# Kernel tuning notes

Hardware: AMD Instinct MI355X
Metric: run time of the kernel (lower is better)

## Reference

```python
import jax, jax.numpy as jnp
import numpy as np

DIMS = [3, 64, 64, 64, 3]  # [input_dim] + hidden dims + [input_dim]
TOTAL_W = sum(DIMS[l] * DIMS[l + 1] + 4 * DIMS[l + 1] for l in range(len(DIMS) - 1))  # 9356


def setup_inputs() -> dict:
    key = jax.random.key(0)
    k1, k2, k3 = jax.random.split(key, 3)
    B, N = 64, 8192
    context = jax.random.normal(k1, (B, N), dtype=jnp.float32)
    y = jax.random.normal(k2, (B, N, DIMS[0]), dtype=jnp.float32)
    tnw = jax.random.normal(k3, (B, TOTAL_W), dtype=jnp.float32) * 0.1
    return {"context": context, "y": y, "target_networks_weights": tnw}


def reference(context, y, target_networks_weights):
    B = target_networks_weights.shape[0]
    dx = y  # [B, N, dims[0]]
    i = 0
    n_layers = len(DIMS) - 1
    for l in range(n_layers):
        dl, dl1 = DIMS[l], DIMS[l + 1]
        W = target_networks_weights[:, i:i + dl * dl1].reshape(B, dl, dl1)
        i += dl * dl1
        bias = target_networks_weights[:, i:i + dl1]          # [B, dl1]
        i += dl1
        w_scale = target_networks_weights[:, i:i + dl1]        # [B, dl1]
        i += dl1
        b_scale = target_networks_weights[:, i:i + dl1]        # [B, dl1]
        i += dl1
        w_shift = target_networks_weights[:, i:i + dl1]        # [B, dl1]
        i += dl1
        # batched matmul + bias
        dx = jnp.einsum('bnd,bde->bne', dx, W) + bias[:, None, :]
        # sigmoid gate: bmm(context[:, :, None], w_scale[:, None, :]) = outer product
        scale = jax.nn.sigmoid(context[:, :, None] * w_scale[:, None, :] + b_scale[:, None, :])
        dx = scale * dx
        # shift term
        dx = dx + context[:, :, None] * w_shift[:, None, :]
        if l < n_layers - 1:
            dx = jax.nn.softplus(dx)
    return dx
```

## Files before the change

### kernel.cpp

```cpp
#include <hip/hip_runtime.h>
#include <math.h>

#define BB 64
#define NN 8192
#define TOTAL_W 9356

typedef _Float16 f16x8 __attribute__((ext_vector_type(8)));
typedef float f32x4 __attribute__((ext_vector_type(4)));
typedef float f32x2 __attribute__((ext_vector_type(2)));
typedef unsigned int u32x2 __attribute__((ext_vector_type(2)));

#define L2E 1.44269504088896340736f
#define LN2 0.6931471805599453f

#define W0_OFF   0
#define FILM_OFF 768
#define A1_OFF   (FILM_OFF + 4096)
#define A2_OFF   (A1_OFF + 8192)
#define ACT_OFF  (A2_OFF + 8192)
#define LDS_BYTES (ACT_OFF + 256*128)

#define MFMA16(a, b, c) __builtin_amdgcn_mfma_f32_16x16x32_f16(a, b, c, 0, 0, 0)
#define EXP2 __builtin_amdgcn_exp2f
#define LOG2 __builtin_amdgcn_logf
#define RCPF __builtin_amdgcn_rcpf

__device__ __forceinline__ f32x2 pfma(f32x2 a, f32x2 b, f32x2 c) {
  return __builtin_elementwise_fma(a, b, c);
}

__device__ __forceinline__ f32x4 filmq(const unsigned char* smem, int l, int prm, int q) {
  return *(const f32x4*)(smem + FILM_OFF + (((l * 4 + prm) * 64 + q) << 2));
}

template<bool SP>
__device__ __forceinline__ u32x2 film_quad(f32x4 acc, float ctx,
                                           f32x4 wscq, f32x4 bscq, f32x4 wshq) {
  f32x2 ctx2 = {ctx, ctx};
  f32x2 one = {1.f, 1.f};
  f32x2 z0 = pfma(ctx2, (f32x2){wscq.x, wscq.y}, (f32x2){bscq.x, bscq.y});
  f32x2 z1 = pfma(ctx2, (f32x2){wscq.z, wscq.w}, (f32x2){bscq.z, bscq.w});
  f32x2 d0 = {EXP2(-z0.x), EXP2(-z0.y)};  d0 += one;
  f32x2 d1 = {EXP2(-z1.x), EXP2(-z1.y)};  d1 += one;
  f32x2 s0 = {RCPF(d0.x), RCPF(d0.y)};
  f32x2 s1 = {RCPF(d1.x), RCPF(d1.y)};
  f32x2 v0 = pfma(ctx2, (f32x2){wshq.x, wshq.y}, s0 * (f32x2){acc.x, acc.y});
  f32x2 v1 = pfma(ctx2, (f32x2){wshq.z, wshq.w}, s1 * (f32x2){acc.z, acc.w});
  if (SP) {
    f32x2 l2 = {L2E, L2E}, ln = {LN2, LN2};
    f32x2 t0 = v0 * l2, t1 = v1 * l2;
    f32x2 u0 = {EXP2(t0.x), EXP2(t0.y)};  u0 += one;
    f32x2 u1 = {EXP2(t1.x), EXP2(t1.y)};  u1 += one;
    f32x2 g0 = {LOG2(u0.x), LOG2(u0.y)};
    f32x2 g1 = {LOG2(u1.x), LOG2(u1.y)};
    v0 = g0 * ln;
    v1 = g1 * ln;
  }
  auto p01 = __builtin_amdgcn_cvt_pkrtz(v0.x, v0.y);
  auto p23 = __builtin_amdgcn_cvt_pkrtz(v1.x, v1.y);
  u32x2 w;
  w.x = __builtin_bit_cast(unsigned int, p01);
  w.y = __builtin_bit_cast(unsigned int, p23);
  return w;
}

__device__ __forceinline__ void act_store(unsigned char* smem, int pt, int slot, u32x2 w) {
  int pos = ((((slot >> 1) ^ (pt & 7)) << 1) | (slot & 1));
  *(u32x2*)(smem + ACT_OFF + pt * 128 + (pos << 3)) = w;
}
__device__ __forceinline__ f16x8 act_load(const unsigned char* smem, int pt, int pair) {
  int gr = pair ^ (pt & 7);
  return *(const f16x8*)(smem + ACT_OFF + pt * 128 + (gr << 4));
}

__global__ __launch_bounds__(512, 6)
void ode_hypernet_kernel(const float* __restrict__ context,
                         const float* __restrict__ y,
                         const float* __restrict__ tnw,
                         float* __restrict__ out) {
  __shared__ __align__(16) unsigned char smem[LDS_BYTES];
  const int b = blockIdx.y;
  const int tid = threadIdx.x;
  const float* __restrict__ wb = tnw + (size_t)b * TOTAL_W;

  if (tid < 192) ((float*)(smem + W0_OFF))[tid] = wb[tid];
  if (tid < 64) {
    const int biaso[4] = {192, 4544, 8896, 9344};
    const int dim[4] = {64, 64, 64, 3};
#pragma unroll
    for (int l = 0; l < 4; ++l) {
      float bv = 0.f, wscv = 0.f, bscv = 0.f, wshv = 0.f;
      if (tid < dim[l]) {
        int bo = biaso[l], d = dim[l];
        bv = wb[bo + tid];
        wscv = wb[bo + d + tid] * L2E;
        bscv = wb[bo + 2 * d + tid] * L2E;
        wshv = wb[bo + 3 * d + tid];
      }
      float* f = (float*)(smem + FILM_OFF) + l * 256;
      f[tid] = bv;
      f[64 + tid] = wscv;
      f[128 + tid] = bscv;
      f[192 + tid] = wshv;
    }
  }
#pragma unroll
  for (int L = 0; L < 2; ++L) {
    const int woff = L ? 4800 : 448;
    const int aoff = L ? A2_OFF : A1_OFF;
#pragma unroll
    for (int it = 0; it < 2; ++it) {
      int idx = tid + it * 512;
      int f_in = idx >> 4;
      int q = idx & 15;
      f32x4 w4 = *(const f32x4*)(wb + woff + f_in * 64 + q * 4);
      int m = q >> 2;
      int c4 = (q & 3) * 4;
      int t = f_in >> 5;
      int h = (f_in >> 3) & 3;
      int i = f_in & 7;
      unsigned char* base = smem + aoff + (m * 128 + t * 64 + h * 16 + c4) * 16 + i * 2;
#pragma unroll
      for (int j = 0; j < 4; ++j)
        *(_Float16*)(base + j * 16) = (_Float16)w4[j];
    }
  }
  const int lane = tid & 63;
  const int colA = lane & 15;
  const int hA = lane >> 4;
  f16x8 A3r0, A3r1;
#pragma unroll
  for (int i = 0; i < 8; ++i) {
    A3r0[i] = (colA < 3) ? (_Float16)wb[9152 + (8 * hA + i) * 3 + colA] : (_Float16)0.f;
    A3r1[i] = (colA < 3) ? (_Float16)wb[9152 + (32 + 8 * hA + i) * 3 + colA] : (_Float16)0.f;
  }
  __syncthreads();

  const int wid = tid >> 6;
  const int g = lane >> 4;
  const int col = lane & 15;
  const int pt0 = wid * 32 + col;
  const int pt1 = pt0 + 16;
  const int q4 = 4 * g;

#pragma unroll 1
  for (int ss = 0; ss < 2; ++ss) {
    const int nbase = blockIdx.x * 512 + ss * 256;
    const int n0 = nbase + pt0, n1 = nbase + pt1;
    const float ctx0 = context[(size_t)b * NN + n0];
    const float ctx1 = context[(size_t)b * NN + n1];
    const size_t yb0 = ((size_t)b * NN + n0) * 3;
    const size_t yb1 = ((size_t)b * NN + n1) * 3;
    const float y00 = y[yb0], y01 = y[yb0 + 1], y02 = y[yb0 + 2];
    const float y10 = y[yb1], y11 = y[yb1 + 1], y12 = y[yb1 + 2];

#pragma unroll
    for (int m = 0; m < 4; ++m) {
      const int q = 16 * m + q4;
      f32x4 biasq = filmq(smem, 0, 0, q);
      f32x4 w0a = *(const f32x4*)(smem + W0_OFF + ((0 * 64 + q) << 2));
      f32x4 w0b = *(const f32x4*)(smem + W0_OFF + ((1 * 64 + q) << 2));
      f32x4 w0c = *(const f32x4*)(smem + W0_OFF + ((2 * 64 + q) << 2));
      f32x2 aLo, aHi, cLo, cHi;
      aLo = pfma((f32x2){y00, y00}, (f32x2){w0a.x, w0a.y}, (f32x2){biasq.x, biasq.y});
      aLo = pfma((f32x2){y01, y01}, (f32x2){w0b.x, w0b.y}, aLo);
      aLo = pfma((f32x2){y02, y02}, (f32x2){w0c.x, w0c.y}, aLo);
      aHi = pfma((f32x2){y00, y00}, (f32x2){w0a.z, w0a.w}, (f32x2){biasq.z, biasq.w});
      aHi = pfma((f32x2){y01, y01}, (f32x2){w0b.z, w0b.w}, aHi);
      aHi = pfma((f32x2){y02, y02}, (f32x2){w0c.z, w0c.w}, aHi);
      cLo = pfma((f32x2){y10, y10}, (f32x2){w0a.x, w0a.y}, (f32x2){biasq.x, biasq.y});
      cLo = pfma((f32x2){y11, y11}, (f32x2){w0b.x, w0b.y}, cLo);
      cLo = pfma((f32x2){y12, y12}, (f32x2){w0c.x, w0c.y}, cLo);
      cHi = pfma((f32x2){y10, y10}, (f32x2){w0a.z, w0a.w}, (f32x2){biasq.z, biasq.w});
      cHi = pfma((f32x2){y11, y11}, (f32x2){w0b.z, w0b.w}, cHi);
      cHi = pfma((f32x2){y12, y12}, (f32x2){w0c.z, w0c.w}, cHi);
      f32x4 acc0 = {aLo.x, aLo.y, aHi.x, aHi.y};
      f32x4 acc1 = {cLo.x, cLo.y, cHi.x, cHi.y};
      f32x4 wscq = filmq(smem, 0, 1, q);
      f32x4 bscq = filmq(smem, 0, 2, q);
      f32x4 wshq = filmq(smem, 0, 3, q);
      act_store(smem, pt0, 4 * m + g, film_quad<true>(acc0, ctx0, wscq, bscq, wshq));
      act_store(smem, pt1, 4 * m + g, film_quad<true>(acc1, ctx1, wscq, bscq, wshq));
    }

#pragma unroll
    for (int L = 1; L <= 2; ++L) {
      const int aoff = (L == 1) ? A1_OFF : A2_OFF;
      f16x8 B00 = act_load(smem, pt0, g);
      f16x8 B01 = act_load(smem, pt0, 4 + g);
      f16x8 B10 = act_load(smem, pt1, g);
      f16x8 B11 = act_load(smem, pt1, 4 + g);
#pragma unroll
      for (int m = 0; m < 4; ++m) {
        const int q = 16 * m + q4;
        f32x4 biasq = filmq(smem, L, 0, q);
        f16x8 a0 = *(const f16x8*)(smem + aoff + ((m * 2 + 0) * 64 + lane) * 16);
        f16x8 a1 = *(const f16x8*)(smem + aoff + ((m * 2 + 1) * 64 + lane) * 16);
        f32x4 c0 = biasq, c1 = biasq;
        c0 = MFMA16(a0, B00, c0);
        c0 = MFMA16(a1, B01, c0);
        c1 = MFMA16(a0, B10, c1);
        c1 = MFMA16(a1, B11, c1);
        f32x4 wscq = filmq(smem, L, 1, q);
        f32x4 bscq = filmq(smem, L, 2, q);
        f32x4 wshq = filmq(smem, L, 3, q);
        act_store(smem, pt0, 4 * m + g, film_quad<true>(c0, ctx0, wscq, bscq, wshq));
        act_store(smem, pt1, 4 * m + g, film_quad<true>(c1, ctx1, wscq, bscq, wshq));
      }
    }

    {
      f16x8 B00 = act_load(smem, pt0, g);
      f16x8 B01 = act_load(smem, pt0, 4 + g);
      f16x8 B10 = act_load(smem, pt1, g);
      f16x8 B11 = act_load(smem, pt1, 4 + g);
      f32x4 biasq = filmq(smem, 3, 0, q4);
      f32x4 c0 = biasq, c1 = biasq;
      c0 = MFMA16(A3r0, B00, c0);
      c0 = MFMA16(A3r1, B01, c0);
      c1 = MFMA16(A3r0, B10, c1);
      c1 = MFMA16(A3r1, B11, c1);
      f32x4 wscq = filmq(smem, 3, 1, q4);
      f32x4 bscq = filmq(smem, 3, 2, q4);
      f32x4 wshq = filmq(smem, 3, 3, q4);
      if (g == 0) {
#pragma unroll
        for (int p = 0; p < 2; ++p) {
          f32x4 c = p ? c1 : c0;
          float ctx = p ? ctx1 : ctx0;
          int n = p ? n1 : n0;
#pragma unroll
          for (int j = 0; j < 3; ++j) {
            float z = fmaf(ctx, wscq[j], bscq[j]);
            float s = RCPF(1.0f + EXP2(-z));
            float v = fmaf(ctx, wshq[j], s * c[j]);
            out[((size_t)b * NN + n) * 3 + j] = v;
          }
        }
      }
    }
  }
}

extern "C" void kernel_launch(void* const* d_in, const int* in_sizes, int n_in,
                              void* d_out, int out_size, void* d_ws, size_t ws_size,
                              hipStream_t stream) {
  const float* context = (const float*)d_in[0];
  const float* y       = (const float*)d_in[1];
  const float* tnw     = (const float*)d_in[2];
  float* out           = (float*)d_out;

  dim3 grid(NN / 512, BB, 1);
  dim3 block(512, 1, 1);
  ode_hypernet_kernel<<<grid, block, 0, stream>>>(context, y, tnw, out);
}
```

Baseline: 53.28 us.

## Use MFMA for first layer, shrink blocks to 256 threads, interleave FiLM params

Replaces the scalar packed-FMA first layer with an MFMA that takes zero-padded fp16 y inputs and W0 held in registers. It interleaves the FiLM parameters so each quad reads bias, scale and shift from one contiguous 64-byte chunk, and hoists all context and y loads ahead of the loop. Blocks shrink from 512 to 256 threads over half as many points each (so twice as many blocks), with a smaller activation LDS buffer and a launch bound without a min-blocks hint. The cost is fp16 rounding of the y inputs and first-layer weights, more per-block weight-setup overhead since each block redoes it for fewer points, and possibly different occupancy.

```diff
diff --git a/kernel.cpp b/kernel.cpp
--- a/kernel.cpp
+++ b/kernel.cpp
@@ -13,12 +13,11 @@
 #define L2E 1.44269504088896340736f
 #define LN2 0.6931471805599453f
 
-#define W0_OFF   0
-#define FILM_OFF 768
-#define A1_OFF   (FILM_OFF + 4096)
-#define A2_OFF   (A1_OFF + 8192)
-#define ACT_OFF  (A2_OFF + 8192)
-#define LDS_BYTES (ACT_OFF + 256*128)
+#define FILM2_OFF 0
+#define A1_OFF    4096
+#define A2_OFF    (A1_OFF + 8192)
+#define ACT_OFF   (A2_OFF + 8192)
+#define LDS_BYTES (ACT_OFF + 128 * 128)
 
 #define MFMA16(a, b, c) __builtin_amdgcn_mfma_f32_16x16x32_f16(a, b, c, 0, 0, 0)
 #define EXP2 __builtin_amdgcn_exp2f
@@ -29,8 +28,8 @@
   return __builtin_elementwise_fma(a, b, c);
 }
 
-__device__ __forceinline__ f32x4 filmq(const unsigned char* smem, int l, int prm, int q) {
-  return *(const f32x4*)(smem + FILM_OFF + (((l * 4 + prm) * 64 + q) << 2));
+__device__ __forceinline__ const f32x4* film_base(const unsigned char* smem, int l, int qd) {
+  return (const f32x4*)(smem + FILM2_OFF + ((l * 16 + qd) << 6));
 }
 
 template<bool SP>
@@ -73,7 +72,7 @@
   return *(const f16x8*)(smem + ACT_OFF + pt * 128 + (gr << 4));
 }
 
-__global__ __launch_bounds__(512, 6)
+__global__ __launch_bounds__(256)
 void ode_hypernet_kernel(const float* __restrict__ context,
                          const float* __restrict__ y,
                          const float* __restrict__ tnw,
@@ -83,7 +82,11 @@
   const int tid = threadIdx.x;
   const float* __restrict__ wb = tnw + (size_t)b * TOTAL_W;
 
-  if (tid < 192) ((float*)(smem + W0_OFF))[tid] = wb[tid];
+  const int lane = tid & 63;
+  const int wid = tid >> 6;
+  const int g = lane >> 4;
+  const int col = lane & 15;
+
   if (tid < 64) {
     const int biaso[4] = {192, 4544, 8896, 9344};
     const int dim[4] = {64, 64, 64, 3};
@@ -97,11 +100,11 @@
         bscv = wb[bo + 2 * d + tid] * L2E;
         wshv = wb[bo + 3 * d + tid];
       }
-      float* f = (float*)(smem + FILM_OFF) + l * 256;
-      f[tid] = bv;
-      f[64 + tid] = wscv;
-      f[128 + tid] = bscv;
-      f[192 + tid] = wshv;
+      float* f2 = (float*)(smem + FILM2_OFF + ((l * 16 + (tid >> 2)) << 6)) + (tid & 3);
+      f2[0] = bv;
+      f2[4] = wscv;
+      f2[8] = bscv;
+      f2[12] = wshv;
     }
   }
 #pragma unroll
@@ -109,8 +112,8 @@
     const int woff = L ? 4800 : 448;
     const int aoff = L ? A2_OFF : A1_OFF;
 #pragma unroll
-    for (int it = 0; it < 2; ++it) {
-      int idx = tid + it * 512;
+    for (int it = 0; it < 4; ++it) {
+      int idx = tid + it * 256;
       int f_in = idx >> 4;
       int q = idx & 15;
       f32x4 w4 = *(const f32x4*)(wb + woff + f_in * 64 + q * 4);
@@ -125,62 +128,61 @@
         *(_Float16*)(base + j * 16) = (_Float16)w4[j];
     }
   }
-  const int lane = tid & 63;
-  const int colA = lane & 15;
-  const int hA = lane >> 4;
+  f16x8 A0r[4];
+#pragma unroll
+  for (int m = 0; m < 4; ++m) {
+#pragma unroll
+    for (int i = 0; i < 8; ++i)
+      A0r[m][i] = (g == 0 && i < 3) ? (_Float16)wb[i * 64 + 16 * m + col] : (_Float16)0.f;
+  }
   f16x8 A3r0, A3r1;
 #pragma unroll
   for (int i = 0; i < 8; ++i) {
-    A3r0[i] = (colA < 3) ? (_Float16)wb[9152 + (8 * hA + i) * 3 + colA] : (_Float16)0.f;
-    A3r1[i] = (colA < 3) ? (_Float16)wb[9152 + (32 + 8 * hA + i) * 3 + colA] : (_Float16)0.f;
+    A3r0[i] = (col < 3) ? (_Float16)wb[9152 + (8 * g + i) * 3 + col] : (_Float16)0.f;
+    A3r1[i] = (col < 3) ? (_Float16)wb[9152 + (32 + 8 * g + i) * 3 + col] : (_Float16)0.f;
   }
   __syncthreads();
 
-  const int wid = tid >> 6;
-  const int g = lane >> 4;
-  const int col = lane & 15;
   const int pt0 = wid * 32 + col;
   const int pt1 = pt0 + 16;
-  const int q4 = 4 * g;
-
-#pragma unroll 1
+
+  const int nb = blockIdx.x * 256;
+  const size_t cb = (size_t)b * NN;
+  float ctxs[4], yv[4][3];
+#pragma unroll
+  for (int k = 0; k < 4; ++k) {
+    int n = nb + (k >> 1) * 128 + pt0 + (k & 1) * 16;
+    ctxs[k] = context[cb + n];
+    const float* yp = y + (cb + n) * 3;
+    yv[k][0] = yp[0]; yv[k][1] = yp[1]; yv[k][2] = yp[2];
+  }
+
+#pragma unroll
   for (int ss = 0; ss < 2; ++ss) {
-    const int nbase = blockIdx.x * 512 + ss * 256;
-    const int n0 = nbase + pt0, n1 = nbase + pt1;
-    const float ctx0 = context[(size_t)b * NN + n0];
-    const float ctx1 = context[(size_t)b * NN + n1];
-    const size_t yb0 = ((size_t)b * NN + n0) * 3;
-    const size_t yb1 = ((size_t)b * NN + n1) * 3;
-    const float y00 = y[yb0], y01 = y[yb0 + 1], y02 = y[yb0 + 2];
-    const float y10 = y[yb1], y11 = y[yb1 + 1], y12 = y[yb1 + 2];
+    const float ctx0 = ctxs[ss * 2], ctx1 = ctxs[ss * 2 + 1];
+    const int n0 = nb + ss * 128 + pt0;
+    const int n1 = n0 + 16;
+
+    f16x8 By0 = {0, 0, 0, 0, 0, 0, 0, 0};
+    f16x8 By1 = {0, 0, 0, 0, 0, 0, 0, 0};
+    if (g == 0) {
+      By0[0] = (_Float16)yv[ss * 2][0];
+      By0[1] = (_Float16)yv[ss * 2][1];
+      By0[2] = (_Float16)yv[ss * 2][2];
+      By1[0] = (_Float16)yv[ss * 2 + 1][0];
+      By1[1] = (_Float16)yv[ss * 2 + 1][1];
+      By1[2] = (_Float16)yv[ss * 2 + 1][2];
+    }
 
 #pragma unroll
     for (int m = 0; m < 4; ++m) {
-      const int q = 16 * m + q4;
-      f32x4 biasq = filmq(smem, 0, 0, q);
-      f32x4 w0a = *(const f32x4*)(smem + W0_OFF + ((0 * 64 + q) << 2));
-      f32x4 w0b = *(const f32x4*)(smem + W0_OFF + ((1 * 64 + q) << 2));
-      f32x4 w0c = *(const f32x4*)(smem + W0_OFF + ((2 * 64 + q) << 2));
-      f32x2 aLo, aHi, cLo, cHi;
-      aLo = pfma((f32x2){y00, y00}, (f32x2){w0a.x, w0a.y}, (f32x2){biasq.x, biasq.y});
-      aLo = pfma((f32x2){y01, y01}, (f32x2){w0b.x, w0b.y}, aLo);
-      aLo = pfma((f32x2){y02, y02}, (f32x2){w0c.x, w0c.y}, aLo);
-      aHi = pfma((f32x2){y00, y00}, (f32x2){w0a.z, w0a.w}, (f32x2){biasq.z, biasq.w});
-      aHi = pfma((f32x2){y01, y01}, (f32x2){w0b.z, w0b.w}, aHi);
-      aHi = pfma((f32x2){y02, y02}, (f32x2){w0c.z, w0c.w}, aHi);
-      cLo = pfma((f32x2){y10, y10}, (f32x2){w0a.x, w0a.y}, (f32x2){biasq.x, biasq.y});
-      cLo = pfma((f32x2){y11, y11}, (f32x2){w0b.x, w0b.y}, cLo);
-      cLo = pfma((f32x2){y12, y12}, (f32x2){w0c.x, w0c.y}, cLo);
-      cHi = pfma((f32x2){y10, y10}, (f32x2){w0a.z, w0a.w}, (f32x2){biasq.z, biasq.w});
-      cHi = pfma((f32x2){y11, y11}, (f32x2){w0b.z, w0b.w}, cHi);
-      cHi = pfma((f32x2){y12, y12}, (f32x2){w0c.z, w0c.w}, cHi);
-      f32x4 acc0 = {aLo.x, aLo.y, aHi.x, aHi.y};
-      f32x4 acc1 = {cLo.x, cLo.y, cHi.x, cHi.y};
-      f32x4 wscq = filmq(smem, 0, 1, q);
-      f32x4 bscq = filmq(smem, 0, 2, q);
-      f32x4 wshq = filmq(smem, 0, 3, q);
-      act_store(smem, pt0, 4 * m + g, film_quad<true>(acc0, ctx0, wscq, bscq, wshq));
-      act_store(smem, pt1, 4 * m + g, film_quad<true>(acc1, ctx1, wscq, bscq, wshq));
+      const f32x4* fb = film_base(smem, 0, 4 * m + g);
+      f32x4 biasq = fb[0], wscq = fb[1], bscq = fb[2], wshq = fb[3];
+      f32x4 c0 = biasq, c1 = biasq;
+      c0 = MFMA16(A0r[m], By0, c0);
+      c1 = MFMA16(A0r[m], By1, c1);
+      act_store(smem, pt0, 4 * m + g, film_quad<true>(c0, ctx0, wscq, bscq, wshq));
+      act_store(smem, pt1, 4 * m + g, film_quad<true>(c1, ctx1, wscq, bscq, wshq));
     }
 
 #pragma unroll
@@ -192,8 +194,8 @@
       f16x8 B11 = act_load(smem, pt1, 4 + g);
 #pragma unroll
       for (int m = 0; m < 4; ++m) {
-        const int q = 16 * m + q4;
-        f32x4 biasq = filmq(smem, L, 0, q);
+        const f32x4* fb = film_base(smem, L, 4 * m + g);
+        f32x4 biasq = fb[0], wscq = fb[1], bscq = fb[2], wshq = fb[3];
         f16x8 a0 = *(const f16x8*)(smem + aoff + ((m * 2 + 0) * 64 + lane) * 16);
         f16x8 a1 = *(const f16x8*)(smem + aoff + ((m * 2 + 1) * 64 + lane) * 16);
         f32x4 c0 = biasq, c1 = biasq;
@@ -201,9 +203,6 @@
         c0 = MFMA16(a1, B01, c0);
         c1 = MFMA16(a0, B10, c1);
         c1 = MFMA16(a1, B11, c1);
-        f32x4 wscq = filmq(smem, L, 1, q);
-        f32x4 bscq = filmq(smem, L, 2, q);
-        f32x4 wshq = filmq(smem, L, 3, q);
         act_store(smem, pt0, 4 * m + g, film_quad<true>(c0, ctx0, wscq, bscq, wshq));
         act_store(smem, pt1, 4 * m + g, film_quad<true>(c1, ctx1, wscq, bscq, wshq));
       }
@@ -214,15 +213,13 @@
       f16x8 B01 = act_load(smem, pt0, 4 + g);
       f16x8 B10 = act_load(smem, pt1, g);
       f16x8 B11 = act_load(smem, pt1, 4 + g);
-      f32x4 biasq = filmq(smem, 3, 0, q4);
+      const f32x4* fb = film_base(smem, 3, g);
+      f32x4 biasq = fb[0], wscq = fb[1], bscq = fb[2], wshq = fb[3];
       f32x4 c0 = biasq, c1 = biasq;
       c0 = MFMA16(A3r0, B00, c0);
       c0 = MFMA16(A3r1, B01, c0);
       c1 = MFMA16(A3r0, B10, c1);
       c1 = MFMA16(A3r1, B11, c1);
-      f32x4 wscq = filmq(smem, 3, 1, q4);
-      f32x4 bscq = filmq(smem, 3, 2, q4);
-      f32x4 wshq = filmq(smem, 3, 3, q4);
       if (g == 0) {
 #pragma unroll
         for (int p = 0; p < 2; ++p) {
@@ -250,7 +247,7 @@
   const float* tnw     = (const float*)d_in[2];
   float* out           = (float*)d_out;
 
-  dim3 grid(NN / 512, BB, 1);
-  dim3 block(512, 1, 1);
+  dim3 grid(NN / 256, BB, 1);
+  dim3 block(256, 1, 1);
   ode_hypernet_kernel<<<grid, block, 0, stream>>>(context, y, tnw, out);
 }
```

Result: slower. 55.64 us (+4.4%).
